# Kernel tuning notes

Measured on AMD Instinct MI355X. Metric: run time of the kernel, lower is better.

## Reference

```python
import jax, jax.numpy as jnp
import numpy as np

B, S, D_MODEL, HEAD, D_KV = 8, 1024, 1024, 16, 64


def setup_inputs() -> dict:
    key = jax.random.key(0)
    ks = jax.random.split(key, 10)
    std = 1.0 / np.sqrt(D_MODEL)
    inp = {
        "queries": jax.random.normal(ks[0], (B, S, D_MODEL), jnp.float32),
        "keys": jax.random.normal(ks[1], (B, S, D_MODEL), jnp.float32),
        "values": jax.random.normal(ks[2], (B, S, D_MODEL), jnp.float32),
        "group_prob": jax.random.uniform(ks[3], (B, 1, S, S), jnp.float32),
        "attention_mask": jax.random.randint(ks[4], (B, 1, S, S), 0, 2, jnp.int32),
        "Wq": jax.random.normal(ks[5], (HEAD * D_KV, D_MODEL), jnp.float32) * std,
        "bq": jnp.zeros((HEAD * D_KV,), jnp.float32),
        "Wk": jax.random.normal(ks[6], (HEAD * D_KV, D_MODEL), jnp.float32) * std,
        "bk": jnp.zeros((HEAD * D_KV,), jnp.float32),
        "Wv": jax.random.normal(ks[7], (HEAD * D_KV, D_MODEL), jnp.float32) * std,
        "bv": jnp.zeros((HEAD * D_KV,), jnp.float32),
    }
    return inp


def reference(queries, keys, values, group_prob, attention_mask, Wq, bq, Wk, bk, Wv, bv):
    b, nq = queries.shape[:2]
    # QKV projections -> [b, head, seq, d_kv]
    q = (queries @ Wq.T + bq).reshape(b, nq, HEAD, D_KV).transpose(0, 2, 1, 3)
    k = (keys @ Wk.T + bk).reshape(b, -1, HEAD, D_KV).transpose(0, 2, 1, 3)
    v = (values @ Wv.T + bv).reshape(b, -1, HEAD, D_KV).transpose(0, 2, 1, 3)
    # scaled scores [b, head, nq, nk]
    att = jnp.einsum("bhqd,bhkd->bhqk", q, k) / np.sqrt(D_KV).astype(np.float32)
    # NOTE: the original torch code calls att.masked_fill(...) (out-of-place)
    # and discards the result, so attention_mask has no effect. Replicated here.
    att = jax.nn.softmax(att, axis=-1)
    att = att * group_prob  # post-softmax group scaling (breaks fused SDPA)
    out = jnp.einsum("bhqk,bhkd->bhqd", att, v)
    return out.transpose(0, 2, 1, 3).reshape(b, nq, HEAD * D_KV)
```

## Files before the change

kernel.cpp:

```cpp
#include <hip/hip_runtime.h>

#define B_SZ 8
#define S_SZ 1024
#define DM   1024
#define NH   16
#define DK   64

typedef __bf16 bf16;
typedef __bf16 bf16x8 __attribute__((ext_vector_type(8)));
typedef float  f32x4  __attribute__((ext_vector_type(4)));

__device__ __forceinline__ f32x4 mfma16x16x32(bf16x8 a, bf16x8 b, f32x4 c) {
    return __builtin_amdgcn_mfma_f32_16x16x32_bf16(a, b, c, 0, 0, 0);
}

typedef const __attribute__((address_space(1))) void* gptr_t;
typedef __attribute__((address_space(3))) void*       sptr_t;
__device__ __forceinline__ void async_cp16(const void* g, void* s) {
    __builtin_amdgcn_global_load_lds((gptr_t)g, (sptr_t)s, 16, 0, 0);
}

__global__ __launch_bounds__(256)
void cvt_kernel(const float* __restrict__ x0, const float* __restrict__ x1,
                const float* __restrict__ x2, const float* __restrict__ w0,
                const float* __restrict__ w1, const float* __restrict__ w2,
                bf16* __restrict__ xb, bf16* __restrict__ wb)
{
    const int z = blockIdx.y;
    const float* src;
    bf16* dst;
    int n;
    if (z < 3) {
        src = (z == 0) ? x0 : (z == 1) ? x1 : x2;
        dst = xb + (size_t)z * (8u * 1024 * 1024);
        n = 8 * 1024 * 1024;
    } else {
        const int w = z - 3;
        src = (w == 0) ? w0 : (w == 1) ? w1 : w2;
        dst = wb + (size_t)w * (1024 * 1024);
        n = 1024 * 1024;
    }
    const int idx = (blockIdx.x * 256 + threadIdx.x) * 8;
    if (idx >= n) return;
    const float4 a = *(const float4*)(src + idx);
    const float4 c = *(const float4*)(src + idx + 4);
    union { bf16 h[8]; uint4 u; } pk;
    pk.h[0] = (bf16)a.x; pk.h[1] = (bf16)a.y; pk.h[2] = (bf16)a.z; pk.h[3] = (bf16)a.w;
    pk.h[4] = (bf16)c.x; pk.h[5] = (bf16)c.y; pk.h[6] = (bf16)c.z; pk.h[7] = (bf16)c.w;
    *(uint4*)(dst + idx) = pk.u;
}

__global__ __launch_bounds__(256)
void cvt_gp_kernel(const float* __restrict__ gp, bf16* __restrict__ gpb)
{
    const int idx = (blockIdx.x * 256 + threadIdx.x) * 8;
    const float4 a = *(const float4*)(gp + idx);
    const float4 c = *(const float4*)(gp + idx + 4);
    union { bf16 h[8]; uint4 u; } pk;
    pk.h[0] = (bf16)a.x; pk.h[1] = (bf16)a.y; pk.h[2] = (bf16)a.z; pk.h[3] = (bf16)a.w;
    pk.h[4] = (bf16)c.x; pk.h[5] = (bf16)c.y; pk.h[6] = (bf16)c.z; pk.h[7] = (bf16)c.w;
    *(uint4*)(gpb + idx) = pk.u;
}

__global__ __launch_bounds__(256, 2)
void qkv_gemm(const bf16* __restrict__ xb, const bf16* __restrict__ wb,
              const float* __restrict__ bq, const float* __restrict__ bk,
              const float* __restrict__ bv,
              bf16* __restrict__ qb, bf16* __restrict__ kb,
              bf16* __restrict__ vb)
{
    const int z = blockIdx.z;
    const bf16* A  = xb + (size_t)z * (8u * 1024 * 1024);
    const bf16* Bm = wb + (size_t)z * (1024 * 1024);
    const float* bias = (z == 0) ? bq : (z == 1) ? bk : bv;

    __shared__ bf16 Ash[128 * 64];
    __shared__ bf16 Bsh[128 * 64];

    const int tid  = threadIdx.x;
    const int wid  = tid >> 6;
    const int lane = tid & 63;
    const int quad = lane >> 4;
    const int l16  = lane & 15;
    const int wm   = wid >> 1, wn = wid & 1;
    const int bm   = blockIdx.x, bn = blockIdx.y;

    f32x4 acc[4][4] = {};

    for (int k0 = 0; k0 < DM; k0 += 64) {
        __syncthreads();
        #pragma unroll
        for (int i = 0; i < 4; ++i) {
            const int e   = (i * 256 + tid) * 8;
            const int row = e >> 6;
            const int c   = ((e >> 3) & 7) ^ (row & 7);
            async_cp16(A  + (size_t)(bm * 128 + row) * DM + k0 + c * 8, &Ash[e]);
            async_cp16(Bm + (size_t)(bn * 128 + row) * DM + k0 + c * 8, &Bsh[e]);
        }
        __syncthreads();

        #pragma unroll
        for (int ks = 0; ks < 2; ++ks) {
            bf16x8 af[4], bfr[4];
            #pragma unroll
            for (int mi = 0; mi < 4; ++mi) {
                const int row = wm * 64 + mi * 16 + l16;
                af[mi] = *(const bf16x8*)&Ash[row * 64 + (((ks * 4 + quad) ^ (l16 & 7)) << 3)];
            }
            #pragma unroll
            for (int ni = 0; ni < 4; ++ni) {
                const int row = wn * 64 + ni * 16 + l16;
                bfr[ni] = *(const bf16x8*)&Bsh[row * 64 + (((ks * 4 + quad) ^ (l16 & 7)) << 3)];
            }
            #pragma unroll
            for (int mi = 0; mi < 4; ++mi)
                #pragma unroll
                for (int ni = 0; ni < 4; ++ni)
                    acc[mi][ni] = mfma16x16x32(af[mi], bfr[ni], acc[mi][ni]);
        }
    }

    #pragma unroll
    for (int ni = 0; ni < 4; ++ni) {
        const int n    = bn * 128 + wn * 64 + ni * 16 + l16;
        const float bv_ = bias[n];
        const int h = n >> 6, d = n & 63;
        #pragma unroll
        for (int mi = 0; mi < 4; ++mi) {
            const int m0 = bm * 128 + wm * 64 + mi * 16 + quad * 4;
            const int b  = m0 >> 10;
            const int s0 = m0 & 1023;
            if (z == 2) {
                union { bf16 h4[4]; uint2 u; } pk;
                #pragma unroll
                for (int r = 0; r < 4; ++r) pk.h4[r] = (bf16)(acc[mi][ni][r] + bv_);
                *(uint2*)(vb + ((size_t)((b * NH + h) * DK + d)) * S_SZ + s0) = pk.u;
            } else {
                bf16* dst      = (z == 0) ? qb : kb;
                const float sc = (z == 0) ? 0.125f : 1.0f;
                #pragma unroll
                for (int r = 0; r < 4; ++r)
                    dst[((size_t)(b * NH + h) * S_SZ + (s0 + r)) * DK + d] =
                        (bf16)((acc[mi][ni][r] + bv_) * sc);
            }
        }
    }
}

__global__ __launch_bounds__(256, 3)
void attn_kernel(const bf16* __restrict__ qb, const bf16* __restrict__ kb,
                 const bf16* __restrict__ vb, const bf16* __restrict__ gpb,
                 float* __restrict__ out)
{
    __shared__ bf16 Ksh[128 * 64];
    __shared__ bf16 Vsh[64 * 128];
    __shared__ bf16 Psh[4][16 * 136];
    __shared__ float Lsh[4][16];

    const int tid  = threadIdx.x;
    const int wid  = tid >> 6;
    const int lane = tid & 63;
    const int quad = lane >> 4;
    const int l16  = lane & 15;

    const int bh = blockIdx.x;
    const int qt = blockIdx.y;
    const int b  = bh >> 4;
    const int h  = bh & (NH - 1);
    const int q0 = qt * 64 + wid * 16;

    const bf16* qr = qb + ((size_t)bh * S_SZ + q0 + l16) * DK;
    const bf16x8 qf0 = *(const bf16x8*)(qr + quad * 8);
    const bf16x8 qf1 = *(const bf16x8*)(qr + 32 + quad * 8);

    f32x4 acc[4] = {};
    float lpart = 0.0f;

    const bf16* gpq = gpb + ((size_t)b * S_SZ + q0 + l16) * S_SZ;

    for (int kt = 0; kt < S_SZ / 128; ++kt) {
        __syncthreads();
        #pragma unroll
        for (int i = 0; i < 4; ++i) {
            const int e   = (i * 256 + tid) * 8;
            const int row = e >> 6;
            const int c   = ((e >> 3) & 7) ^ (row & 7);
            async_cp16(kb + (size_t)bh * (S_SZ * DK) + (size_t)(kt * 128 + row) * DK + c * 8,
                       &Ksh[e]);
        }
        #pragma unroll
        for (int i = 0; i < 4; ++i) {
            const int e   = (i * 256 + tid) * 8;
            const int row = e >> 7;
            const int c   = ((e >> 3) & 15) ^ (row & 15);
            async_cp16(vb + ((size_t)bh * DK + row) * S_SZ + kt * 128 + c * 8, &Vsh[e]);
        }
        ushort4 gpl[8];
        #pragma unroll
        for (int nb = 0; nb < 8; ++nb)
            gpl[nb] = *(const ushort4*)(gpq + kt * 128 + nb * 16 + quad * 4);
        __syncthreads();

        f32x4 sc[8];
        #pragma unroll
        for (int nb = 0; nb < 8; ++nb) {
            const int row = nb * 16 + l16;
            const bf16x8 kf0 = *(const bf16x8*)&Ksh[row * 64 + ((quad ^ (l16 & 7)) << 3)];
            const bf16x8 kf1 = *(const bf16x8*)&Ksh[row * 64 + (((4 + quad) ^ (l16 & 7)) << 3)];
            f32x4 s = {0.0f, 0.0f, 0.0f, 0.0f};
            s = mfma16x16x32(kf0, qf0, s);
            s = mfma16x16x32(kf1, qf1, s);
            sc[nb] = s;
        }

        #pragma unroll
        for (int nb = 0; nb < 8; ++nb) {
            union { bf16 h4[4]; uint2 u; } pk;
            const unsigned short* gu = (const unsigned short*)&gpl[nb];
            #pragma unroll
            for (int r = 0; r < 4; ++r) {
                const float pv = __expf(sc[nb][r]);
                lpart += pv;
                const float g = __uint_as_float(((unsigned)gu[r]) << 16);
                pk.h4[r] = (bf16)(pv * g);
            }
            *(uint2*)&Psh[wid][l16 * 136 + nb * 16 + quad * 4] = pk.u;
        }

        bf16x8 pf[4];
        #pragma unroll
        for (int j = 0; j < 4; ++j)
            pf[j] = *(const bf16x8*)&Psh[wid][l16 * 136 + j * 32 + quad * 8];
        #pragma unroll
        for (int ni = 0; ni < 4; ++ni) {
            const int vrow = ni * 16 + l16;
            #pragma unroll
            for (int j = 0; j < 4; ++j) {
                const bf16x8 vf = *(const bf16x8*)&Vsh[vrow * 128 + (((j * 4 + quad) ^ l16) << 3)];
                acc[ni] = mfma16x16x32(pf[j], vf, acc[ni]);
            }
        }
    }

    lpart += __shfl_xor(lpart, 16, 64);
    lpart += __shfl_xor(lpart, 32, 64);
    if (quad == 0) Lsh[wid][l16] = 1.0f / lpart;
    __syncthreads();

    #pragma unroll
    for (int r = 0; r < 4; ++r) {
        const float inv = Lsh[wid][quad * 4 + r];
        float* orow = out + ((size_t)b * S_SZ + q0 + quad * 4 + r) * DM + h * DK;
        #pragma unroll
        for (int ni = 0; ni < 4; ++ni)
            orow[ni * 16 + l16] = acc[ni][r] * inv;
    }
}

extern "C" void kernel_launch(void* const* d_in, const int* in_sizes, int n_in,
                              void* d_out, int out_size, void* d_ws, size_t ws_size,
                              hipStream_t stream) {
    const float* queries = (const float*)d_in[0];
    const float* keys    = (const float*)d_in[1];
    const float* values  = (const float*)d_in[2];
    const float* gp      = (const float*)d_in[3];
    const float* Wq = (const float*)d_in[5];
    const float* bq = (const float*)d_in[6];
    const float* Wk = (const float*)d_in[7];
    const float* bk = (const float*)d_in[8];
    const float* Wv = (const float*)d_in[9];
    const float* bv = (const float*)d_in[10];
    float* out = (float*)d_out;

    bf16* xb = (bf16*)d_ws;
    bf16* wb = xb + (size_t)3 * 8 * 1024 * 1024;
    bf16* qb = wb + (size_t)3 * 1024 * 1024;
    bf16* kb = qb + (size_t)B_SZ * NH * S_SZ * DK;
    bf16* vb = kb + (size_t)B_SZ * NH * S_SZ * DK;
    bf16* gpb = xb;
    (void)ws_size; (void)in_sizes; (void)n_in; (void)out_size;

    dim3 gc(4096, 6);
    cvt_kernel<<<gc, 256, 0, stream>>>(queries, keys, values, Wq, Wk, Wv, xb, wb);

    dim3 g1(64, 8, 3);
    qkv_gemm<<<g1, 256, 0, stream>>>(xb, wb, bq, bk, bv, qb, kb, vb);

    cvt_gp_kernel<<<dim3(4096), 256, 0, stream>>>(gp, gpb);

    dim3 g2(B_SZ * NH , S_SZ / 64 , 1);
    attn_kernel<<<g2, 256, 0, stream>>>(qb, kb, vb, gpb, out);
}
```

Baseline: 358.8 us.

## Split keys across waves with register-resident K/V and LDS cross-wave reduction

Each wave now covers all 64 query rows of the block but only a quarter of the keys (256). K, V and group-prob fragments are loaded straight from global memory into registers instead of being staged through LDS with block-wide barriers. Partial outputs and row sums from the four waves are combined through an LDS union buffer, and the final output is written with float4 stores. This removes per-tile __syncthreads and LDS staging, at the cost of much higher register pressure (64 accumulator floats per lane), uncoalesced 16-byte direct global loads, and a reduction epilogue.

New measurement: 431.1 us. +20.1%, slower.

```diff
diff --git a/kernel.cpp b/kernel.cpp
--- a/kernel.cpp
+++ b/kernel.cpp
@@ -152,10 +152,11 @@
                  const bf16* __restrict__ vb, const bf16* __restrict__ gpb,
                  float* __restrict__ out)
 {
-    __shared__ bf16 Ksh[128 * 64];
-    __shared__ bf16 Vsh[64 * 128];
-    __shared__ bf16 Psh[4][16 * 136];
-    __shared__ float Lsh[4][16];
+    __shared__ float Lsh[4][4][16];
+    __shared__ union SMem {
+        bf16  P[4][64 * 40];
+        float O[2][64][68];
+    } sm;
 
     const int tid  = threadIdx.x;
     const int wid  = tid >> 6;
@@ -167,93 +168,132 @@
     const int qt = blockIdx.y;
     const int b  = bh >> 4;
     const int h  = bh & (NH - 1);
-    const int q0 = qt * 64 + wid * 16;
-
-    const bf16* qr = qb + ((size_t)bh * S_SZ + q0 + l16) * DK;
-    const bf16x8 qf0 = *(const bf16x8*)(qr + quad * 8);
-    const bf16x8 qf1 = *(const bf16x8*)(qr + 32 + quad * 8);
-
-    f32x4 acc[4] = {};
-    float lpart = 0.0f;
-
-    const bf16* gpq = gpb + ((size_t)b * S_SZ + q0 + l16) * S_SZ;
-
-    for (int kt = 0; kt < S_SZ / 128; ++kt) {
-        __syncthreads();
-        #pragma unroll
-        for (int i = 0; i < 4; ++i) {
-            const int e   = (i * 256 + tid) * 8;
-            const int row = e >> 6;
-            const int c   = ((e >> 3) & 7) ^ (row & 7);
-            async_cp16(kb + (size_t)bh * (S_SZ * DK) + (size_t)(kt * 128 + row) * DK + c * 8,
-                       &Ksh[e]);
-        }
-        #pragma unroll
-        for (int i = 0; i < 4; ++i) {
-            const int e   = (i * 256 + tid) * 8;
-            const int row = e >> 7;
-            const int c   = ((e >> 3) & 15) ^ (row & 15);
-            async_cp16(vb + ((size_t)bh * DK + row) * S_SZ + kt * 128 + c * 8, &Vsh[e]);
-        }
-        ushort4 gpl[8];
-        #pragma unroll
-        for (int nb = 0; nb < 8; ++nb)
-            gpl[nb] = *(const ushort4*)(gpq + kt * 128 + nb * 16 + quad * 4);
-        __syncthreads();
-
-        f32x4 sc[8];
-        #pragma unroll
-        for (int nb = 0; nb < 8; ++nb) {
-            const int row = nb * 16 + l16;
-            const bf16x8 kf0 = *(const bf16x8*)&Ksh[row * 64 + ((quad ^ (l16 & 7)) << 3)];
-            const bf16x8 kf1 = *(const bf16x8*)&Ksh[row * 64 + (((4 + quad) ^ (l16 & 7)) << 3)];
-            f32x4 s = {0.0f, 0.0f, 0.0f, 0.0f};
-            s = mfma16x16x32(kf0, qf0, s);
-            s = mfma16x16x32(kf1, qf1, s);
-            sc[nb] = s;
-        }
-
-        #pragma unroll
-        for (int nb = 0; nb < 8; ++nb) {
-            union { bf16 h4[4]; uint2 u; } pk;
-            const unsigned short* gu = (const unsigned short*)&gpl[nb];
-            #pragma unroll
-            for (int r = 0; r < 4; ++r) {
-                const float pv = __expf(sc[nb][r]);
-                lpart += pv;
-                const float g = __uint_as_float(((unsigned)gu[r]) << 16);
-                pk.h4[r] = (bf16)(pv * g);
+    const int q0 = qt * 64;
+
+    const bf16* qbase = qb + ((size_t)bh * S_SZ + q0) * DK;
+    bf16x8 qf[4][2];
+    #pragma unroll
+    for (int m = 0; m < 4; ++m) {
+        const bf16* qr = qbase + (m * 16 + l16) * DK + quad * 8;
+        qf[m][0] = *(const bf16x8*)(qr);
+        qf[m][1] = *(const bf16x8*)(qr + 32);
+    }
+
+    const int key0 = wid * 256;
+    const bf16* kbase  = kb  + (size_t)bh * (S_SZ * DK) + (size_t)key0 * DK;
+    const bf16* vbase  = vb  + (size_t)bh * (DK * S_SZ);
+    const bf16* gpbase = gpb + ((size_t)b * S_SZ + q0) * S_SZ + key0;
+
+    f32x4 acc[4][4] = {};
+    float lp[4] = {};
+
+    bf16* Pw = sm.P[wid];
+
+    #pragma unroll 2
+    for (int kc = 0; kc < 8; ++kc) {
+        const int kb0 = kc * 32;
+
+        bf16x8 kf[2][2];
+        #pragma unroll
+        for (int kt2 = 0; kt2 < 2; ++kt2) {
+            const bf16* kr = kbase + (size_t)(kb0 + kt2 * 16 + l16) * DK + quad * 8;
+            kf[kt2][0] = *(const bf16x8*)(kr);
+            kf[kt2][1] = *(const bf16x8*)(kr + 32);
+        }
+        ushort4 gpl[4][2];
+        #pragma unroll
+        for (int m = 0; m < 4; ++m)
+            #pragma unroll
+            for (int kt2 = 0; kt2 < 2; ++kt2)
+                gpl[m][kt2] = *(const ushort4*)(gpbase + (size_t)(m * 16 + l16) * S_SZ
+                                                + kb0 + kt2 * 16 + quad * 4);
+        bf16x8 vf[4];
+        #pragma unroll
+        for (int n = 0; n < 4; ++n)
+            vf[n] = *(const bf16x8*)(vbase + (size_t)(n * 16 + l16) * S_SZ
+                                     + key0 + kb0 + quad * 8);
+
+        #pragma unroll
+        for (int m = 0; m < 4; ++m) {
+            #pragma unroll
+            for (int kt2 = 0; kt2 < 2; ++kt2) {
+                f32x4 s = {0.0f, 0.0f, 0.0f, 0.0f};
+                s = mfma16x16x32(kf[kt2][0], qf[m][0], s);
+                s = mfma16x16x32(kf[kt2][1], qf[m][1], s);
+                union { bf16 h4[4]; uint2 u; } pk;
+                const unsigned short* gu = (const unsigned short*)&gpl[m][kt2];
+                #pragma unroll
+                for (int r = 0; r < 4; ++r) {
+                    const float pv = __expf(s[r]);
+                    lp[m] += pv;
+                    const float g = __uint_as_float(((unsigned)gu[r]) << 16);
+                    pk.h4[r] = (bf16)(pv * g);
+                }
+                *(uint2*)&Pw[(m * 16 + l16) * 40 + kt2 * 16 + quad * 4] = pk.u;
             }
-            *(uint2*)&Psh[wid][l16 * 136 + nb * 16 + quad * 4] = pk.u;
-        }
-
-        bf16x8 pf[4];
-        #pragma unroll
-        for (int j = 0; j < 4; ++j)
-            pf[j] = *(const bf16x8*)&Psh[wid][l16 * 136 + j * 32 + quad * 8];
-        #pragma unroll
-        for (int ni = 0; ni < 4; ++ni) {
-            const int vrow = ni * 16 + l16;
-            #pragma unroll
-            for (int j = 0; j < 4; ++j) {
-                const bf16x8 vf = *(const bf16x8*)&Vsh[vrow * 128 + (((j * 4 + quad) ^ l16) << 3)];
-                acc[ni] = mfma16x16x32(pf[j], vf, acc[ni]);
-            }
-        }
-    }
-
-    lpart += __shfl_xor(lpart, 16, 64);
-    lpart += __shfl_xor(lpart, 32, 64);
-    if (quad == 0) Lsh[wid][l16] = 1.0f / lpart;
+        }
+
+        #pragma unroll
+        for (int m = 0; m < 4; ++m) {
+            const bf16x8 pf = *(const bf16x8*)&Pw[(m * 16 + l16) * 40 + quad * 8];
+            #pragma unroll
+            for (int n = 0; n < 4; ++n)
+                acc[m][n] = mfma16x16x32(pf, vf[n], acc[m][n]);
+        }
+    }
+
+    #pragma unroll
+    for (int m = 0; m < 4; ++m) {
+        lp[m] += __shfl_xor(lp[m], 16, 64);
+        lp[m] += __shfl_xor(lp[m], 32, 64);
+    }
+    if (quad == 0) {
+        #pragma unroll
+        for (int m = 0; m < 4; ++m) Lsh[wid][m][l16] = lp[m];
+    }
     __syncthreads();
 
+    float (*OA)[68] = sm.O[0];
+    float (*OB)[68] = sm.O[1];
+    if (wid & 1) {
+        float (*O)[68] = (wid == 1) ? OA : OB;
+        #pragma unroll
+        for (int m = 0; m < 4; ++m)
+            #pragma unroll
+            for (int n = 0; n < 4; ++n)
+                #pragma unroll
+                for (int r = 0; r < 4; ++r)
+                    O[m * 16 + quad * 4 + r][n * 16 + l16] = acc[m][n][r];
+    }
+    __syncthreads();
+    if (!(wid & 1)) {
+        float (*O)[68] = (wid == 0) ? OA : OB;
+        #pragma unroll
+        for (int m = 0; m < 4; ++m)
+            #pragma unroll
+            for (int n = 0; n < 4; ++n)
+                #pragma unroll
+                for (int r = 0; r < 4; ++r)
+                    O[m * 16 + quad * 4 + r][n * 16 + l16] += acc[m][n][r];
+    }
+    __syncthreads();
+
+    const int rr  = lane >> 2;
+    const int row = wid * 16 + rr;
+    const float invl = 1.0f / (Lsh[0][wid][rr] + Lsh[1][wid][rr] +
+                               Lsh[2][wid][rr] + Lsh[3][wid][rr]);
+    float* orow = out + ((size_t)b * S_SZ + q0 + row) * DM + h * DK;
     #pragma unroll
-    for (int r = 0; r < 4; ++r) {
-        const float inv = Lsh[wid][quad * 4 + r];
-        float* orow = out + ((size_t)b * S_SZ + q0 + quad * 4 + r) * DM + h * DK;
-        #pragma unroll
-        for (int ni = 0; ni < 4; ++ni)
-            orow[ni * 16 + l16] = acc[ni][r] * inv;
+    for (int c = 0; c < 4; ++c) {
+        const int col = c * 16 + (lane & 3) * 4;
+        const float4 a4 = *(const float4*)&OA[row][col];
+        const float4 b4 = *(const float4*)&OB[row][col];
+        float4 o;
+        o.x = (a4.x + b4.x) * invl;
+        o.y = (a4.y + b4.y) * invl;
+        o.z = (a4.z + b4.z) * invl;
+        o.w = (a4.w + b4.w) * invl;
+        *(float4*)(orow + col) = o;
     }
 }
 
```

## Double-buffer K/V tiles in attention with 64-key steps and prefetch

Applied to the files above, without the earlier changes.

The attention loop now uses 64-key tiles with two LDS buffers for K and V instead of a single 128-key buffer. The next tile's async K/V copies and its group_prob register loads are issued before computing on the current tile, so load latency can overlap the MFMA and softmax work. Keys per iteration are halved, but the number of barriers per key stays the same, since the old pre-load barrier is dropped. LDS use also falls slightly. The risk is that each barrier still drains every outstanding load, which limits how much overlap is gained, and the smaller tiles leave less independent work per step.

Result: no change. 354.3 us (-1.3%).

```diff
diff --git a/kernel.cpp b/kernel.cpp
--- a/kernel.cpp
+++ b/kernel.cpp
@@ -152,9 +152,9 @@
                  const bf16* __restrict__ vb, const bf16* __restrict__ gpb,
                  float* __restrict__ out)
 {
-    __shared__ bf16 Ksh[128 * 64];
-    __shared__ bf16 Vsh[64 * 128];
-    __shared__ bf16 Psh[4][16 * 136];
+    __shared__ bf16 Ksh[2][64 * 64];
+    __shared__ bf16 Vsh[2][64 * 64];
+    __shared__ bf16 Psh[4][16 * 72];
     __shared__ float Lsh[4][16];
 
     const int tid  = threadIdx.x;
@@ -177,69 +177,88 @@
     float lpart = 0.0f;
 
     const bf16* gpq = gpb + ((size_t)b * S_SZ + q0 + l16) * S_SZ;
-
-    for (int kt = 0; kt < S_SZ / 128; ++kt) {
-        __syncthreads();
-        #pragma unroll
-        for (int i = 0; i < 4; ++i) {
+    const bf16* kbh = kb + (size_t)bh * (S_SZ * DK);
+    const bf16* vbh = vb + (size_t)bh * ((size_t)DK * S_SZ);
+
+    auto STAGE = [&](int t, int bufi) {
+        #pragma unroll
+        for (int i = 0; i < 2; ++i) {
             const int e   = (i * 256 + tid) * 8;
             const int row = e >> 6;
             const int c   = ((e >> 3) & 7) ^ (row & 7);
-            async_cp16(kb + (size_t)bh * (S_SZ * DK) + (size_t)(kt * 128 + row) * DK + c * 8,
-                       &Ksh[e]);
-        }
-        #pragma unroll
-        for (int i = 0; i < 4; ++i) {
+            async_cp16(kbh + (size_t)(t * 64 + row) * DK + c * 8, &Ksh[bufi][e]);
+        }
+        #pragma unroll
+        for (int i = 0; i < 2; ++i) {
             const int e   = (i * 256 + tid) * 8;
-            const int row = e >> 7;
-            const int c   = ((e >> 3) & 15) ^ (row & 15);
-            async_cp16(vb + ((size_t)bh * DK + row) * S_SZ + kt * 128 + c * 8, &Vsh[e]);
-        }
-        ushort4 gpl[8];
-        #pragma unroll
-        for (int nb = 0; nb < 8; ++nb)
-            gpl[nb] = *(const ushort4*)(gpq + kt * 128 + nb * 16 + quad * 4);
-        __syncthreads();
-
-        f32x4 sc[8];
-        #pragma unroll
-        for (int nb = 0; nb < 8; ++nb) {
+            const int row = e >> 6;
+            const int c   = ((e >> 3) & 7) ^ (row & 7);
+            async_cp16(vbh + (size_t)row * S_SZ + t * 64 + c * 8, &Vsh[bufi][e]);
+        }
+    };
+    auto GPLOAD = [&](int t, ushort4 (&g)[4]) {
+        #pragma unroll
+        for (int nb = 0; nb < 4; ++nb)
+            g[nb] = *(const ushort4*)(gpq + t * 64 + nb * 16 + quad * 4);
+    };
+    auto COMPUTE = [&](const bf16* Kb, const bf16* Vb, const ushort4 (&g)[4]) {
+        f32x4 sc[4];
+        #pragma unroll
+        for (int nb = 0; nb < 4; ++nb) {
             const int row = nb * 16 + l16;
-            const bf16x8 kf0 = *(const bf16x8*)&Ksh[row * 64 + ((quad ^ (l16 & 7)) << 3)];
-            const bf16x8 kf1 = *(const bf16x8*)&Ksh[row * 64 + (((4 + quad) ^ (l16 & 7)) << 3)];
+            const bf16x8 kf0 = *(const bf16x8*)&Kb[row * 64 + ((quad ^ (l16 & 7)) << 3)];
+            const bf16x8 kf1 = *(const bf16x8*)&Kb[row * 64 + (((4 + quad) ^ (l16 & 7)) << 3)];
             f32x4 s = {0.0f, 0.0f, 0.0f, 0.0f};
             s = mfma16x16x32(kf0, qf0, s);
             s = mfma16x16x32(kf1, qf1, s);
             sc[nb] = s;
         }
-
-        #pragma unroll
-        for (int nb = 0; nb < 8; ++nb) {
+        #pragma unroll
+        for (int nb = 0; nb < 4; ++nb) {
             union { bf16 h4[4]; uint2 u; } pk;
-            const unsigned short* gu = (const unsigned short*)&gpl[nb];
+            const unsigned short* gu = (const unsigned short*)&g[nb];
             #pragma unroll
             for (int r = 0; r < 4; ++r) {
                 const float pv = __expf(sc[nb][r]);
                 lpart += pv;
-                const float g = __uint_as_float(((unsigned)gu[r]) << 16);
-                pk.h4[r] = (bf16)(pv * g);
-            }
-            *(uint2*)&Psh[wid][l16 * 136 + nb * 16 + quad * 4] = pk.u;
-        }
-
-        bf16x8 pf[4];
-        #pragma unroll
-        for (int j = 0; j < 4; ++j)
-            pf[j] = *(const bf16x8*)&Psh[wid][l16 * 136 + j * 32 + quad * 8];
+                const float gg = __uint_as_float(((unsigned)gu[r]) << 16);
+                pk.h4[r] = (bf16)(pv * gg);
+            }
+            *(uint2*)&Psh[wid][l16 * 72 + nb * 16 + quad * 4] = pk.u;
+        }
+        bf16x8 pf[2];
+        #pragma unroll
+        for (int j = 0; j < 2; ++j)
+            pf[j] = *(const bf16x8*)&Psh[wid][l16 * 72 + j * 32 + quad * 8];
         #pragma unroll
         for (int ni = 0; ni < 4; ++ni) {
             const int vrow = ni * 16 + l16;
             #pragma unroll
-            for (int j = 0; j < 4; ++j) {
-                const bf16x8 vf = *(const bf16x8*)&Vsh[vrow * 128 + (((j * 4 + quad) ^ l16) << 3)];
+            for (int j = 0; j < 2; ++j) {
+                const bf16x8 vf =
+                    *(const bf16x8*)&Vb[vrow * 64 + (((j * 4 + quad) ^ (l16 & 7)) << 3)];
                 acc[ni] = mfma16x16x32(pf[j], vf, acc[ni]);
             }
         }
+    };
+
+    ushort4 gplA[4], gplB[4];
+    STAGE(0, 0);
+    GPLOAD(0, gplA);
+    __syncthreads();
+
+    for (int tt = 0; tt < 8; ++tt) {
+        const int t0 = tt * 2;
+        STAGE(t0 + 1, 1);
+        GPLOAD(t0 + 1, gplB);
+        COMPUTE(Ksh[0], Vsh[0], gplA);
+        __syncthreads();
+        if (t0 + 2 < 16) {
+            STAGE(t0 + 2, 0);
+            GPLOAD(t0 + 2, gplA);
+        }
+        COMPUTE(Ksh[1], Vsh[1], gplB);
+        __syncthreads();
     }
 
     lpart += __shfl_xor(lpart, 16, 64);
```
